# Kernel tuning notes

Hardware: AMD Instinct MI355X
Metric: run time of the kernel (lower is better)

Reference implementation:

```python
import jax, jax.numpy as jnp
import numpy as np

B, S, F, D, NH, K, NB = 128, 200, 32, 512, 4, 4, 2
Dh = D // NH
UP = 704  # round(1.3*512) up to multiple of 64
FD = 7    # forecast_days
EPS = 1e-5


def _layernorm(x, w):
    mu = x.mean(-1, keepdims=True)
    var = ((x - mu) ** 2).mean(-1, keepdims=True)
    return (x - mu) / jnp.sqrt(var + EPS) * w


def _forward(x, w_in, b_in, ln1_w, conv_w, conv_b, w_gates, r_gates, b_gates,
             gn_w, ln2_w, ff_up, ff_down, post_ln_w, fc1_w, fc1_b, fc2_w, fc2_b):
    b, s, _ = x.shape
    h = x @ w_in + b_in  # (B,S,D) input projection
    for blk in range(NB):
        xn = _layernorm(h, ln1_w[blk])
        # causal depthwise conv1d (kernel K) + swish, feeds i/f gates
        xp = jnp.pad(xn, ((0, 0), (K - 1, 0), (0, 0)))
        xc = conv_b[blk] + sum(conv_w[blk, k] * xp[:, k:k + s, :] for k in range(K))
        xc = xc * jax.nn.sigmoid(xc)  # swish
        xch = xc.reshape(b, s, NH, Dh)
        xnh = xn.reshape(b, s, NH, Dh)
        # headwise (block-diagonal) gate projections
        ipre = jnp.einsum('bshd,hde->bshe', xch, w_gates[blk, 0])
        fpre = jnp.einsum('bshd,hde->bshe', xch, w_gates[blk, 1])
        zpre = jnp.einsum('bshd,hde->bshe', xnh, w_gates[blk, 2])
        opre = jnp.einsum('bshd,hde->bshe', xnh, w_gates[blk, 3])
        pre = jnp.stack([ipre, fpre, zpre, opre], 0)        # (4,B,S,NH,Dh)
        pre = jnp.transpose(pre, (2, 0, 1, 3, 4))           # (S,4,B,NH,Dh)
        R = r_gates[blk]                                     # (4,NH,Dh,Dh)
        bg = b_gates[blk].reshape(4, NH, Dh)

        def step(carry, g):
            hs, cs, ns, ms = carry  # each (B,NH,Dh)
            rec = jnp.einsum('bhd,ghde->gbhe', hs, R)
            iraw = g[0] + rec[0] + bg[0]
            fraw = g[1] + rec[1] + bg[1]
            zraw = g[2] + rec[2] + bg[2]
            oraw = g[3] + rec[3] + bg[3]
            # stabilized exponential gating (vanilla sLSTM backend)
            logf = ms + jax.nn.log_sigmoid(fraw)
            m_new = jnp.maximum(iraw, logf)
            ig = jnp.exp(iraw - m_new)
            fg = jnp.exp(logf - m_new)
            c_new = fg * cs + ig * jnp.tanh(zraw)
            n_new = fg * ns + ig
            h_new = jax.nn.sigmoid(oraw) * c_new / n_new
            return (h_new, c_new, n_new, m_new), h_new

        z0 = jnp.zeros((b, NH, Dh), x.dtype)
        _, hseq = jax.lax.scan(step, (z0, z0, z0, z0), pre)  # (S,B,NH,Dh)
        # multi-head groupnorm (per head, over Dh)
        mu = hseq.mean(-1, keepdims=True)
        var = ((hseq - mu) ** 2).mean(-1, keepdims=True)
        y = (hseq - mu) / jnp.sqrt(var + EPS) * gn_w[blk].reshape(NH, Dh)
        y = jnp.transpose(y, (1, 0, 2, 3)).reshape(b, s, D)
        h = h + y  # residual
        # gated GeLU feedforward with residual
        xn2 = _layernorm(h, ln2_w[blk])
        u = xn2 @ ff_up[blk]                                 # (B,S,2*UP)
        gate, up = jnp.split(u, 2, -1)
        h = h + (jax.nn.gelu(gate) * up) @ ff_down[blk]
    h = _layernorm(h, post_ln_w)  # post-blocks norm
    last = h[:, -1, :]
    out = jax.nn.relu(last @ fc1_w + fc1_b) @ fc2_w + fc2_b  # (B,FD)
    return out


def setup_inputs() -> dict:
    key = jax.random.key(0)
    ks = jax.random.split(key, 12)

    def rn(k, shape, s=0.02):
        return jax.random.normal(k, shape, jnp.float32) * s

    return {
        'x': jax.random.normal(ks[0], (B, S, F), jnp.float32),
        'w_in': rn(ks[1], (F, D), 0.1),
        'b_in': jnp.zeros((D,), jnp.float32),
        'ln1_w': jnp.ones((NB, D), jnp.float32),
        'conv_w': rn(ks[2], (NB, K, D), 0.1),
        'conv_b': jnp.zeros((NB, D), jnp.float32),
        'w_gates': rn(ks[3], (NB, 4, NH, Dh, Dh), 0.05),
        'r_gates': rn(ks[4], (NB, 4, NH, Dh, Dh), 0.05),
        'b_gates': rn(ks[5], (NB, 4, D), 0.1),
        'gn_w': jnp.ones((NB, D), jnp.float32),
        'ln2_w': jnp.ones((NB, D), jnp.float32),
        'ff_up': rn(ks[6], (NB, D, 2 * UP), 0.05),
        'ff_down': rn(ks[7], (NB, UP, D), 0.05),
        'post_ln_w': jnp.ones((D,), jnp.float32),
        'fc1_w': rn(ks[8], (D, D // 2), 0.05),
        'fc1_b': jnp.zeros((D // 2,), jnp.float32),
        'fc2_w': rn(ks[9], (D // 2, FD), 0.05),
        'fc2_b': jnp.zeros((FD,), jnp.float32),
    }


def reference(x, w_in, b_in, ln1_w, conv_w, conv_b, w_gates, r_gates, b_gates,
              gn_w, ln2_w, ff_up, ff_down, post_ln_w, fc1_w, fc1_b, fc2_w, fc2_b):
    return _forward(x, w_in, b_in, ln1_w, conv_w, conv_b, w_gates, r_gates, b_gates,
                    gn_w, ln2_w, ff_up, ff_down, post_ln_w, fc1_w, fc1_b, fc2_w, fc2_b)
```

## Files before the change

### kernel.cpp

```cpp
#include <hip/hip_runtime.h>

#define B_  128
#define S_  200
#define F_  32
#define D_  512
#define NH_ 4
#define DH_ 128
#define KK_ 4
#define NB_ 2
#define UP_ 704
#define FD_ 7
#define M_  (B_*S_)

typedef unsigned short u16;
typedef _Float16 f16;
typedef __attribute__((ext_vector_type(8))) _Float16 f16x8;
typedef __attribute__((ext_vector_type(8))) short  s16x8;
typedef __attribute__((ext_vector_type(4))) float  f32x4;

__device__ __forceinline__ u16 f2bf(float f){
  unsigned x = __builtin_bit_cast(unsigned, f);
  return (u16)((x + 0x7fffu + ((x>>16)&1u)) >> 16);
}
__device__ __forceinline__ float bf2f(u16 u){
  return __builtin_bit_cast(float, (unsigned)u << 16);
}
__device__ __forceinline__ f32x4 mfma16(s16x8 a, s16x8 b, f32x4 c){
  return __builtin_amdgcn_mfma_f32_16x16x32_bf16(a, b, c, 0, 0, 0);
}
__device__ __forceinline__ f32x4 mfma16h(f16x8 a, f16x8 b, f32x4 c){
  return __builtin_amdgcn_mfma_f32_16x16x32_f16(a, b, c, 0, 0, 0);
}
__device__ __forceinline__ float frcp(float x){ return __builtin_amdgcn_rcpf(x); }
__device__ __forceinline__ float tanh_fast(float z){
  const float u = __expf(-2.f*fabsf(z));
  const float t = (1.f-u)*frcp(1.f+u);
  return copysignf(t, z);
}
__device__ __forceinline__ float logsig_fast(float f){
  const float t = __expf(-fabsf(f));
  return fminf(f, 0.f) - __logf(1.f + t);
}
__device__ __forceinline__ float sigmoid_fast(float x){
  return frcp(1.f + __expf(-x));
}
__device__ __forceinline__ void bar_lgkm(){
  __builtin_amdgcn_sched_barrier(0);
  asm volatile("s_waitcnt lgkmcnt(0)" ::: "memory");
  __builtin_amdgcn_s_barrier();
  __builtin_amdgcn_sched_barrier(0);
}
template<int CTRL>
__device__ __forceinline__ float dpp_add(float v){
  int x = __builtin_amdgcn_update_dpp(0, __builtin_bit_cast(int, v), CTRL, 0xf, 0xf, false);
  return v + __builtin_bit_cast(float, x);
}
__device__ __forceinline__ float wave_sum64(float v){
  v = dpp_add<0x111>(v);
  v = dpp_add<0x112>(v);
  v = dpp_add<0x114>(v);
  v = dpp_add<0x118>(v);
  v = dpp_add<0x142>(v);
  v = dpp_add<0x143>(v);
  return __builtin_bit_cast(float, __builtin_amdgcn_readlane(__builtin_bit_cast(int, v), 63));
}

__global__ void k_zero(float* __restrict__ p, int n){
  int i = blockIdx.x*256 + threadIdx.x;
  if (i < n) p[i] = 0.f;
}
__global__ void k_sentinel(float* __restrict__ out, int n){
  int i = blockIdx.x*256 + threadIdx.x;
  if (i < n) out[i] = -12345.0f;
}

__global__ void k_cast_pack_gates(const float* __restrict__ in, u16* __restrict__ out, int n){
  int i = blockIdx.x*256 + threadIdx.x;
  if (i >= n) return;
  const int mat = i >> 14;
  const int rem = i & 16383;
  const int slab = rem >> 12;
  const int r2   = rem & 4095;
  const int nn   = r2 >> 5;
  const int kk   = r2 & 31;
  out[i] = f2bf(in[(size_t)mat*16384 + (size_t)(slab*32 + kk)*DH_ + nn]);
}
__global__ void k_cast_pack_up(const float* __restrict__ in, u16* __restrict__ out, int n){
  int i = blockIdx.x*256 + threadIdx.x;
  if (i >= n) return;
  const int per = 512*1408;
  const int blk = i / per;
  const int rem = i - blk*per;
  const int slab = rem / (1408*32);
  const int r2   = rem - slab*(1408*32);
  const int nn   = r2 >> 5;
  const int kk   = r2 & 31;
  const int j = nn & 127, tt = nn >> 7;
  const int col = (j < 64) ? (tt*64 + j) : (UP_ + tt*64 + (j - 64));
  out[i] = f2bf(in[(size_t)(blk*512 + slab*32 + kk)*(2*UP_) + col]);
}
__global__ void k_cast_pack_dn(const float* __restrict__ in, u16* __restrict__ out, int n){
  int i = blockIdx.x*256 + threadIdx.x;
  if (i >= n) return;
  const int per = 704*512;
  const int blk = i / per;
  const int rem = i - blk*per;
  const int slab = rem / (512*32);
  const int r2   = rem - slab*(512*32);
  const int nn   = r2 >> 5;
  const int kk   = r2 & 31;
  out[i] = f2bf(in[(size_t)(blk*704 + slab*32 + kk)*D_ + nn]);
}

__global__ __launch_bounds__(256) void k_inproj(const float* __restrict__ x,
    const float* __restrict__ w, const float* __restrict__ bias, float* __restrict__ h)
{
  __shared__ float xs[8][32];
  const int m0 = blockIdx.x*8, tid = threadIdx.x;
  xs[tid>>5][tid&31] = x[(size_t)(m0 + (tid>>5))*F_ + (tid&31)];
  __syncthreads();
  #pragma unroll
  for (int hf=0; hf<2; ++hf){
    const int e = tid + hf*256;
    float a[8];
    const float bb = bias[e];
    #pragma unroll
    for (int r=0;r<8;r++) a[r]=bb;
    for (int f=0; f<F_; ++f){
      const float wv = w[(size_t)f*D_ + e];
      #pragma unroll
      for (int r=0;r<8;r++) a[r] += xs[r][f]*wv;
    }
    #pragma unroll
    for (int r=0;r<8;r++) h[(size_t)(m0+r)*D_ + e] = a[r];
  }
}

__global__ __launch_bounds__(128) void k_ln(const float* __restrict__ in, const float* __restrict__ w,
      u16* __restrict__ outb)
{
  const int row = blockIdx.x, tid = threadIdx.x;
  const f32x4* rp = (const f32x4*)(in + (size_t)row*D_);
  f32x4 v = rp[tid];
  float s = v[0]+v[1]+v[2]+v[3];
  float q = v[0]*v[0]+v[1]*v[1]+v[2]*v[2]+v[3]*v[3];
  #pragma unroll
  for (int off=32; off; off>>=1){ s += __shfl_down(s,off,64); q += __shfl_down(q,off,64); }
  __shared__ float red[2][2];
  if ((tid&63)==0){ red[tid>>6][0]=s; red[tid>>6][1]=q; }
  __syncthreads();
  const float sum = red[0][0]+red[1][0], sq = red[0][1]+red[1][1];
  const float mu  = sum*(1.f/D_);
  const float var = sq*(1.f/D_) - mu*mu;
  const float inv = rsqrtf(var + 1e-5f);
  f32x4 wv = ((const f32x4*)w)[tid];
  ushort4 ob;
  ob.x=f2bf((v[0]-mu)*inv*wv[0]); ob.y=f2bf((v[1]-mu)*inv*wv[1]);
  ob.z=f2bf((v[2]-mu)*inv*wv[2]); ob.w=f2bf((v[3]-mu)*inv*wv[3]);
  ((ushort4*)(outb + (size_t)row*D_))[tid] = ob;
}

__global__ __launch_bounds__(128) void k_addln(float* __restrict__ h, const u16* __restrict__ y,
      const float* __restrict__ w, u16* __restrict__ outb)
{
  const int row = blockIdx.x, tid = threadIdx.x;
  f32x4 v = ((const f32x4*)(h + (size_t)row*D_))[tid];
  ushort4 yq = ((const ushort4*)(y + (size_t)row*D_))[tid];
  v[0]+=bf2f(yq.x); v[1]+=bf2f(yq.y); v[2]+=bf2f(yq.z); v[3]+=bf2f(yq.w);
  ((f32x4*)(h + (size_t)row*D_))[tid] = v;
  float s = v[0]+v[1]+v[2]+v[3];
  float q = v[0]*v[0]+v[1]*v[1]+v[2]*v[2]+v[3]*v[3];
  #pragma unroll
  for (int off=32; off; off>>=1){ s += __shfl_down(s,off,64); q += __shfl_down(q,off,64); }
  __shared__ float red[2][2];
  if ((tid&63)==0){ red[tid>>6][0]=s; red[tid>>6][1]=q; }
  __syncthreads();
  const float sum = red[0][0]+red[1][0], sq = red[0][1]+red[1][1];
  const float mu  = sum*(1.f/D_);
  const float var = sq*(1.f/D_) - mu*mu;
  const float inv = rsqrtf(var + 1e-5f);
  f32x4 wv = ((const f32x4*)w)[tid];
  ushort4 ob;
  ob.x=f2bf((v[0]-mu)*inv*wv[0]); ob.y=f2bf((v[1]-mu)*inv*wv[1]);
  ob.z=f2bf((v[2]-mu)*inv*wv[2]); ob.w=f2bf((v[3]-mu)*inv*wv[3]);
  ((ushort4*)(outb + (size_t)row*D_))[tid] = ob;
}

__global__ void k_conv(const u16* __restrict__ xnbf, const float* __restrict__ cw,
                       const float* __restrict__ cb, u16* __restrict__ xcc,
                       int s0, int Sc)
{
  const int idx = blockIdx.x*256 + threadIdx.x;
  const int e4 = idx & 127;
  const int sl = (idx >> 7) % Sc;
  const int b  = idx / (128*Sc);
  const int s  = s0 + sl;
  f32x4 acc = ((const f32x4*)cb)[e4];
  #pragma unroll
  for (int k=0;k<KK_;k++){
    const int sp = s - (KK_-1) + k;
    if (sp >= 0){
      f32x4 w4 = ((const f32x4*)cw)[k*128 + e4];
      ushort4 xq = ((const ushort4*)xnbf)[(size_t)(b*S_ + sp)*128 + e4];
      acc[0] += w4[0]*bf2f(xq.x);
      acc[1] += w4[1]*bf2f(xq.y);
      acc[2] += w4[2]*bf2f(xq.z);
      acc[3] += w4[3]*bf2f(xq.w);
    }
  }
  ushort4 o;
  float a;
  a=acc[0]; o.x=f2bf(a*sigmoid_fast(a));
  a=acc[1]; o.y=f2bf(a*sigmoid_fast(a));
  a=acc[2]; o.z=f2bf(a*sigmoid_fast(a));
  a=acc[3]; o.w=f2bf(a*sigmoid_fast(a));
  ((ushort4*)xcc)[idx] = o;
}

__global__ __launch_bounds__(256) void k_gemm_ffn(
    const u16* __restrict__ A, int lda,
    const u16* __restrict__ Bw, int ldb,
    float* __restrict__ C, int ldc,
    int Kdim, int addmode)
{
  __shared__ u16 As[128*40];
  __shared__ u16 Bs[128*40];
  const int tid = threadIdx.x;
  const int m0 = blockIdx.x * 128;
  const int n0 = blockIdx.y * 128;
  const int w = tid >> 6, l = tid & 63;
  const int l16 = l & 15, kg = l >> 4;
  f32x4 acc[2][8];
  #pragma unroll
  for (int i=0;i<2;i++)
    #pragma unroll
    for (int j=0;j<8;j++) acc[i][j] = (f32x4)0.f;
  const int nk = Kdim >> 5;
  for (int kt=0; kt<nk; ++kt){
    const int k0 = kt<<5;
    __syncthreads();
    #pragma unroll
    for (int p=0;p<2;p++){
      const int idx = p*256 + tid;
      const int row = idx>>2, kc = (idx&3)*8;
      s16x8 v = *(const s16x8*)(A + (size_t)(m0+row)*lda + k0 + kc);
      *(s16x8*)&As[row*40 + kc] = v;
    }
    #pragma unroll
    for (int p=0;p<2;p++){
      const int idx = p*256 + tid;
      const int nl = idx>>2, ck = (idx&3)*8;
      s16x8 v = *(const s16x8*)(Bw + (size_t)kt*ldb*32 + (size_t)(n0+nl)*32 + ck);
      *(s16x8*)&Bs[nl*40 + ck] = v;
    }
    __syncthreads();
    s16x8 af[2];
    #pragma unroll
    for (int mf=0;mf<2;mf++)
      af[mf] = *(const s16x8*)&As[(w*32 + mf*16 + l16)*40 + kg*8];
    #pragma unroll
    for (int nf=0;nf<8;nf++){
      s16x8 bfr = *(const s16x8*)&Bs[(nf*16 + l16)*40 + kg*8];
      #pragma unroll
      for (int mf=0;mf<2;mf++)
        acc[mf][nf] = mfma16(af[mf], bfr, acc[mf][nf]);
    }
  }
  #pragma unroll
  for (int mf=0;mf<2;mf++){
    #pragma unroll
    for (int j=0;j<4;j++){
      const int row = m0 + w*32 + mf*16 + kg*4 + j;
      float* cp = C + (size_t)row*ldc + n0 + l16;
      #pragma unroll
      for (int nf=0;nf<8;nf++){
        const float v = acc[mf][nf][j];
        if (addmode) cp[nf*16] += v; else cp[nf*16] = v;
      }
    }
  }
}

__global__ __launch_bounds__(256) void k_gemm_up(
    const u16* __restrict__ A,
    const u16* __restrict__ Bw,
    u16* __restrict__ act)
{
  __shared__ u16 As[128*40];
  __shared__ u16 Bs[128*40];
  const int tid = threadIdx.x;
  const int m0 = blockIdx.x * 128;
  const int n0 = blockIdx.y * 128;
  const int w = tid >> 6, l = tid & 63;
  const int l16 = l & 15, kg = l >> 4;
  f32x4 acc[2][8];
  #pragma unroll
  for (int i=0;i<2;i++)
    #pragma unroll
    for (int j=0;j<8;j++) acc[i][j] = (f32x4)0.f;
  for (int kt=0; kt<16; ++kt){
    const int k0 = kt<<5;
    __syncthreads();
    #pragma unroll
    for (int p=0;p<2;p++){
      const int idx = p*256 + tid;
      const int row = idx>>2, kc = (idx&3)*8;
      s16x8 v = *(const s16x8*)(A + (size_t)(m0+row)*D_ + k0 + kc);
      *(s16x8*)&As[row*40 + kc] = v;
    }
    #pragma unroll
    for (int p=0;p<2;p++){
      const int idx = p*256 + tid;
      const int nl = idx>>2, ck = (idx&3)*8;
      s16x8 v = *(const s16x8*)(Bw + (size_t)kt*(2*UP_)*32 + (size_t)(n0+nl)*32 + ck);
      *(s16x8*)&Bs[nl*40 + ck] = v;
    }
    __syncthreads();
    s16x8 af[2];
    #pragma unroll
    for (int mf=0;mf<2;mf++)
      af[mf] = *(const s16x8*)&As[(w*32 + mf*16 + l16)*40 + kg*8];
    #pragma unroll
    for (int nf=0;nf<8;nf++){
      s16x8 bfr = *(const s16x8*)&Bs[(nf*16 + l16)*40 + kg*8];
      #pragma unroll
      for (int mf=0;mf<2;mf++)
        acc[mf][nf] = mfma16(af[mf], bfr, acc[mf][nf]);
    }
  }
  const int n0h = blockIdx.y * 64;
  #pragma unroll
  for (int mf=0;mf<2;mf++){
    #pragma unroll
    for (int j=0;j<4;j++){
      const int row = m0 + w*32 + mf*16 + kg*4 + j;
      u16* ap = act + (size_t)row*UP_ + n0h + l16;
      #pragma unroll
      for (int nf=0;nf<4;nf++){
        const float gg = acc[mf][nf][j];
        const float uu = acc[mf][nf+4][j];
        const float tt = tanh_fast(0.7978845608028654f*(gg + 0.044715f*gg*gg*gg));
        ap[nf*16] = f2bf(0.5f*gg*(1.f+tt)*uu);
      }
    }
  }
}

__global__ __launch_bounds__(256) void k_gemm_gates(
    const u16* __restrict__ xcc, const u16* __restrict__ xnbf,
    const u16* __restrict__ wg,
    const float* __restrict__ bgates,
    u16* __restrict__ pre, int s0, int Sc)
{
  __shared__ u16 As[128*40];
  __shared__ u16 Bs[128*40];
  const int tid = threadIdx.x;
  const int m0 = blockIdx.x * 128;
  const int gh = blockIdx.y; const int g = gh>>2, hh = gh&3;
  const u16* Bw = wg + (size_t)gh*DH_*DH_;
  const int w = tid >> 6, l = tid & 63;
  const int l16 = l & 15, kg = l >> 4;
  f32x4 acc[2][8];
  #pragma unroll
  for (int i=0;i<2;i++)
    #pragma unroll
    for (int j=0;j<8;j++) acc[i][j] = (f32x4)0.f;
  for (int kt=0; kt<4; ++kt){
    const int k0 = kt<<5;
    __syncthreads();
    #pragma unroll
    for (int p=0;p<2;p++){
      const int idx = p*256 + tid;
      const int row = idx>>2, kc = (idx&3)*8;
      const int m = m0 + row;
      size_t aoff;
      const u16* Abase;
      if (g < 2){ Abase = xcc;  aoff = (size_t)m*D_; }
      else {
        const int b2 = m / Sc, sl2 = m - b2*Sc;
        Abase = xnbf; aoff = (size_t)(b2*S_ + s0 + sl2)*D_;
      }
      s16x8 v = *(const s16x8*)(Abase + aoff + hh*DH_ + k0 + kc);
      *(s16x8*)&As[row*40 + kc] = v;
    }
    #pragma unroll
    for (int p=0;p<2;p++){
      const int idx = p*256 + tid;
      const int nl = idx>>2, ck = (idx&3)*8;
      s16x8 v = *(const s16x8*)(Bw + (size_t)kt*DH_*32 + (size_t)nl*32 + ck);
      *(s16x8*)&Bs[nl*40 + ck] = v;
    }
    __syncthreads();
    s16x8 af[2];
    #pragma unroll
    for (int mf=0;mf<2;mf++)
      af[mf] = *(const s16x8*)&As[(w*32 + mf*16 + l16)*40 + kg*8];
    #pragma unroll
    for (int nf=0;nf<8;nf++){
      s16x8 bfr = *(const s16x8*)&Bs[(nf*16 + l16)*40 + kg*8];
      #pragma unroll
      for (int mf=0;mf<2;mf++)
        acc[mf][nf] = mfma16(af[mf], bfr, acc[mf][nf]);
    }
  }
  #pragma unroll
  for (int mf=0;mf<2;mf++){
    #pragma unroll
    for (int j=0;j<4;j++){
      const int m = m0 + w*32 + mf*16 + kg*4 + j;
      const int b2 = m / Sc;
      const int sl2 = m - b2*Sc;
      #pragma unroll
      for (int nf=0;nf<8;nf++){
        const int col = nf*16 + l16;
        const float bias = bgates[g*D_ + hh*128 + col];
        pre[(((size_t)g*Sc + sl2)*B_ + b2)*D_ + hh*128 + col] =
            __builtin_bit_cast(u16, (f16)(acc[mf][nf][j] + bias));
      }
    }
  }
}

__global__ __launch_bounds__(512, 2) void k_scan(
    const u16* __restrict__ pre,
    const float* __restrict__ rg,
    const float* __restrict__ gnw,
    u16* __restrict__ ybuf,
    float* __restrict__ st, int s0, int Sc)
{
  const int t   = threadIdx.x;
  const int hh  = blockIdx.y;
  const int bg0 = blockIdx.x * 2;
  const int w   = t >> 6;
  const int l   = t & 63;
  const int g   = w >> 1;
  const int ch  = w & 1;
  const int la  = l >> 4, lb = l & 15;

  __shared__ __align__(16) char  hA[16*256];
  __shared__ __align__(16) float recl[16*132];
  __shared__ float red[2][2][2];

  f16x8 Rf[4][4];
  {
    const float* rbase = rg + ((size_t)(g*NH_ + hh)*DH_)*DH_ + ch*64;
    #pragma unroll
    for (int ct=0; ct<4; ++ct)
      #pragma unroll
      for (int ks=0; ks<4; ++ks){
        f16x8 f;
        #pragma unroll
        for (int j=0;j<8;j++)
          f[j] = (f16)rbase[(size_t)(ks*32 + la*8 + j)*DH_ + ct*16 + lb];
        Rf[ct][ks] = f;
      }
  }

  const int pb  = t >> 7;
  const int col = t & 127;
  const int wh  = (t >> 6) & 1;
  const bool act = (pb < 2);
  const int pbc = act ? pb : 0;
  const int SCMP = B_*NH_*DH_;
  const int is  = ((bg0+pbc)*NH_ + hh)*128 + col;

  for (int i = t; i < 16*128; i += 512) ((u16*)hA)[i] = 0;
  float hst=0.f, cst=0.f, nst=0.f, mst=0.f;
  if (act){
    hst = st[0*SCMP + is];
    cst = st[1*SCMP + is];
    nst = st[2*SCMP + is];
    mst = st[3*SCMP + is];
    const int slot = col >> 3;
    *(u16*)&hA[pb*256 + (((slot^pb)&15)<<4) + (col&7)*2] = __builtin_bit_cast(u16, (f16)hst);
  }
  const float gws = gnw[hh*128 + col];
  const u16* prebase = pre + (size_t)(bg0+pbc)*D_ + hh*128 + col;
  const size_t gstride = (size_t)Sc*B_*D_;
  const size_t sstride = (size_t)B_*D_;
  u16 pc16[4]={0,0,0,0}, pn16[4]={0,0,0,0};
  if (act){
    #pragma unroll
    for (int g2=0; g2<4; ++g2)
      pc16[g2] = prebase[g2*gstride];
    const int s1c = (Sc > 1) ? 1 : 0;
    #pragma unroll
    for (int g2=0; g2<4; ++g2)
      pn16[g2] = prebase[g2*gstride + (size_t)s1c*sstride];
  }
  __syncthreads();

  for (int sl=0; sl<Sc; ++sl){
    u16 pl16[4]={0,0,0,0};
    if (act){
      const int sn = (sl+2 < Sc) ? sl+2 : Sc-1;
      #pragma unroll
      for (int g2=0; g2<4; ++g2)
        pl16[g2] = prebase[g2*gstride + (size_t)sn*sstride];
    }

    f32x4 accA[4], accB[4];
    #pragma unroll
    for (int ct=0; ct<4; ++ct){ accA[ct] = (f32x4)0.f; accB[ct] = (f32x4)0.f; }
    #pragma unroll
    for (int ks=0; ks<4; ++ks){
      const int slot = ks*4 + la;
      f16x8 af = *(const f16x8*)&hA[lb*256 + (((slot ^ lb)&15)<<4)];
      if (ks < 2){
        #pragma unroll
        for (int ct=0; ct<4; ++ct) accA[ct] = mfma16h(af, Rf[ct][ks], accA[ct]);
      } else {
        #pragma unroll
        for (int ct=0; ct<4; ++ct) accB[ct] = mfma16h(af, Rf[ct][ks], accB[ct]);
      }
    }
    if (la == 0){
      #pragma unroll
      for (int ct=0; ct<4; ++ct){
        recl[(g*4 + 0)*132 + ch*64 + ct*16 + lb] = accA[ct][0] + accB[ct][0];
        recl[(g*4 + 1)*132 + ch*64 + ct*16 + lb] = accA[ct][1] + accB[ct][1];
      }
    }
    bar_lgkm();

    float hv = 0.f;
    if (act){
      const float iraw = (float)__builtin_bit_cast(f16, pc16[0]) + recl[(0*4+pb)*132 + col];
      const float fraw = (float)__builtin_bit_cast(f16, pc16[1]) + recl[(1*4+pb)*132 + col];
      const float zraw = (float)__builtin_bit_cast(f16, pc16[2]) + recl[(2*4+pb)*132 + col];
      const float oraw = (float)__builtin_bit_cast(f16, pc16[3]) + recl[(3*4+pb)*132 + col];
      const float lf   = mst + logsig_fast(fraw);
      const float mn   = fmaxf(iraw, lf);
      const float ig   = __expf(iraw - mn);
      const float fg   = __expf(lf - mn);
      cst = fg*cst + ig*tanh_fast(zraw);
      nst = fg*nst + ig;
      mst = mn;
      hv = sigmoid_fast(oraw) * cst * frcp(nst);
      hst = hv;
      const int slot = col >> 3;
      *(u16*)&hA[pb*256 + (((slot^pb)&15)<<4) + (col&7)*2] = __builtin_bit_cast(u16, (f16)hv);
      const float s1 = wave_sum64(hv);
      const float s2 = wave_sum64(hv*hv);
      if (l == 0){ red[pb][wh][0] = s1; red[pb][wh][1] = s2; }
    }
    bar_lgkm();

    if (act){
      const float sum = red[pb][0][0] + red[pb][1][0];
      const float sq  = red[pb][0][1] + red[pb][1][1];
      const float mu  = sum * (1.f/128.f);
      const float var = sq * (1.f/128.f) - mu*mu;
      const float y   = (hv - mu) * rsqrtf(var + 1e-5f) * gws;
      ybuf[((size_t)(bg0+pb)*S_ + (s0+sl))*D_ + hh*128 + col] = f2bf(y);
      pc16[0]=pn16[0]; pc16[1]=pn16[1]; pc16[2]=pn16[2]; pc16[3]=pn16[3];
      pn16[0]=pl16[0]; pn16[1]=pl16[1]; pn16[2]=pl16[2]; pn16[3]=pl16[3];
    }
  }
  if (act){
    st[0*SCMP + is] = hst;
    st[1*SCMP + is] = cst;
    st[2*SCMP + is] = nst;
    st[3*SCMP + is] = mst;
  }
}

__global__ __launch_bounds__(256) void k_head(const float* __restrict__ h,
     const float* __restrict__ pw, const float* __restrict__ f1w, const float* __restrict__ f1b,
     const float* __restrict__ f2w, const float* __restrict__ f2bias, float* __restrict__ out)
{
  const int b = blockIdx.x, tid = threadIdx.x;
  __shared__ float nrm[512];
  __shared__ float a1[256];
  __shared__ float red[4][2];
  const float* row = h + ((size_t)b*S_ + (S_-1))*D_;
  const float v0 = row[tid], v1 = row[tid+256];
  float s = v0+v1, q = v0*v0+v1*v1;
  #pragma unroll
  for (int off=32; off; off>>=1){ s += __shfl_down(s,off,64); q += __shfl_down(q,off,64); }
  if ((tid&63)==0){ red[tid>>6][0]=s; red[tid>>6][1]=q; }
  __syncthreads();
  const float sum = red[0][0]+red[1][0]+red[2][0]+red[3][0];
  const float sq  = red[0][1]+red[1][1]+red[2][1]+red[3][1];
  const float mu  = sum*(1.f/D_), var = sq*(1.f/D_) - mu*mu;
  const float inv = rsqrtf(var+1e-5f);
  nrm[tid]      = (v0-mu)*inv*pw[tid];
  nrm[tid+256]  = (v1-mu)*inv*pw[tid+256];
  __syncthreads();
  float acc = f1b[tid];
  for (int d=0; d<D_; ++d) acc += nrm[d]*f1w[(size_t)d*256 + tid];
  a1[tid] = fmaxf(acc, 0.f);
  __syncthreads();
  if (tid < FD_){
    float o = f2bias[tid];
    for (int i=0;i<256;++i) o += a1[i]*f2w[(size_t)i*FD_ + tid];
    out[b*FD_ + tid] = o;
  }
}

extern "C" void kernel_launch(void* const* d_in, const int* in_sizes, int n_in,
                              void* d_out, int out_size, void* d_ws, size_t ws_size,
                              hipStream_t stream)
{
  const float* x       = (const float*)d_in[0];
  const float* w_in    = (const float*)d_in[1];
  const float* b_in    = (const float*)d_in[2];
  const float* ln1_w   = (const float*)d_in[3];
  const float* conv_w  = (const float*)d_in[4];
  const float* conv_b  = (const float*)d_in[5];
  const float* w_gates = (const float*)d_in[6];
  const float* r_gates = (const float*)d_in[7];
  const float* b_gates = (const float*)d_in[8];
  const float* gn_w    = (const float*)d_in[9];
  const float* ln2_w   = (const float*)d_in[10];
  const float* ff_up   = (const float*)d_in[11];
  const float* ff_down = (const float*)d_in[12];
  const float* post_ln = (const float*)d_in[13];
  const float* fc1_w   = (const float*)d_in[14];
  const float* fc1_b   = (const float*)d_in[15];
  const float* fc2_w   = (const float*)d_in[16];
  const float* fc2_b   = (const float*)d_in[17];
  float* out = (float*)d_out;

  char* ws = (char*)d_ws;
  const size_t OFF_H     = 0;
  const size_t OFF_XNBF  = 52428800;
  const size_t OFF_WGBF  = 78643200;
  const size_t OFF_UPBF  = 79691776;
  const size_t OFF_DNBF  = 82575360;
  const size_t OFF_STATE = 84017152;
  const size_t OFF_YBUF  = 85065728;
  const size_t OFF_CHUNK = 111280128;

  if (ws_size < OFF_CHUNK + 655360ull){
    k_sentinel<<<4, 256, 0, stream>>>(out, out_size);
    return;
  }
  const size_t CR = ws_size - OFF_CHUNK;
  int Sc = (int)(CR / 655360ull); if (Sc > S_) Sc = S_;
  int Mc = (int)((CR / 1408ull) & ~(size_t)127); if (Mc > M_) Mc = M_;

  float* h     = (float*)(ws + OFF_H);
  u16*   xnbf  = (u16*)  (ws + OFF_XNBF);
  u16*   wgbf  = (u16*)  (ws + OFF_WGBF);
  u16*   upbf  = (u16*)  (ws + OFF_UPBF);
  u16*   dnbf  = (u16*)  (ws + OFF_DNBF);
  float* st    = (float*)(ws + OFF_STATE);
  u16*   ybuf  = (u16*)  (ws + OFF_YBUF);
  u16*   xcc   = (u16*)  (ws + OFF_CHUNK);
  u16*   prec  = (u16*)  (ws + OFF_CHUNK + (size_t)Sc*131072);
  u16*   actc  = (u16*)  (ws + OFF_CHUNK);

  {
    int n1 = NB_*4*NH_*DH_*DH_;  k_cast_pack_gates<<<(n1+255)/256, 256, 0, stream>>>(w_gates, wgbf, n1);
    int n2 = NB_*D_*2*UP_;       k_cast_pack_up<<<(n2+255)/256, 256, 0, stream>>>(ff_up, upbf, n2);
    int n3 = NB_*UP_*D_;         k_cast_pack_dn<<<(n3+255)/256, 256, 0, stream>>>(ff_down, dnbf, n3);
  }

  k_inproj<<<M_/8, 256, 0, stream>>>(x, w_in, b_in, h);

  for (int blk=0; blk<NB_; ++blk){
    k_ln<<<M_, 128, 0, stream>>>(h, ln1_w + blk*D_, xnbf);
    k_zero<<<1024, 256, 0, stream>>>(st, 4*B_*NH_*DH_);
    for (int s0=0; s0<S_; s0+=Sc){
      const int scur = (S_ - s0 < Sc) ? (S_ - s0) : Sc;
      k_conv<<<scur*64, 256, 0, stream>>>(xnbf, conv_w + blk*KK_*D_, conv_b + blk*D_,
                                          xcc, s0, scur);
      dim3 gg((B_*scur)/128, 16);
      k_gemm_gates<<<gg, 256, 0, stream>>>(xcc, xnbf,
          wgbf + (size_t)blk*4*NH_*DH_*DH_, b_gates + (size_t)blk*4*D_, prec, s0, scur);
      dim3 gs(B_/2, NH_);
      k_scan<<<gs, 512, 0, stream>>>(prec, r_gates + (size_t)blk*4*NH_*DH_*DH_,
                                     gn_w + blk*D_, ybuf, st, s0, scur);
    }
    k_addln<<<M_, 128, 0, stream>>>(h, ybuf, ln2_w + blk*D_, xnbf);
    for (int m0c=0; m0c<M_; m0c+=Mc){
      const int mcur = (M_ - m0c < Mc) ? (M_ - m0c) : Mc;
      dim3 g1(mcur/128, (2*UP_)/128);
      k_gemm_up<<<g1, 256, 0, stream>>>(xnbf + (size_t)m0c*D_,
                                        upbf + (size_t)blk*D_*2*UP_, actc);
      dim3 g2(mcur/128, D_/128);
      k_gemm_ffn<<<g2, 256, 0, stream>>>(actc, UP_,
                                         dnbf + (size_t)blk*UP_*D_, D_,
                                         h + (size_t)m0c*D_, D_, UP_, 1);
    }
  }

  k_head<<<B_, 256, 0, stream>>>(h, post_ln, fc1_w, fc1_b, fc2_w, fc2_b, out);
}
```

Baseline: 979.0 us.

## Process one batch row per scan block and double scan grid size

```diff
diff --git a/kernel.cpp b/kernel.cpp
--- a/kernel.cpp
+++ b/kernel.cpp
@@ -421,7 +421,7 @@
   }
 }
 
-__global__ __launch_bounds__(512, 2) void k_scan(
+__global__ __launch_bounds__(512, 4) void k_scan(
     const u16* __restrict__ pre,
     const float* __restrict__ rg,
     const float* __restrict__ gnw,
@@ -430,7 +430,7 @@
 {
   const int t   = threadIdx.x;
   const int hh  = blockIdx.y;
-  const int bg0 = blockIdx.x * 2;
+  const int bb  = blockIdx.x;
   const int w   = t >> 6;
   const int l   = t & 63;
   const int g   = w >> 1;
@@ -438,8 +438,8 @@
   const int la  = l >> 4, lb = l & 15;
 
   __shared__ __align__(16) char  hA[16*256];
-  __shared__ __align__(16) float recl[16*132];
-  __shared__ float red[2][2][2];
+  __shared__ __align__(16) float recl[4*132];
+  __shared__ float red[2][2];
 
   f16x8 Rf[4][4];
   {
@@ -456,13 +456,11 @@
       }
   }
 
-  const int pb  = t >> 7;
+  const bool act = (t < 128);
   const int col = t & 127;
-  const int wh  = (t >> 6) & 1;
-  const bool act = (pb < 2);
-  const int pbc = act ? pb : 0;
+  const int wh  = t >> 6;
   const int SCMP = B_*NH_*DH_;
-  const int is  = ((bg0+pbc)*NH_ + hh)*128 + col;
+  const int is  = (bb*NH_ + hh)*128 + col;
 
   for (int i = t; i < 16*128; i += 512) ((u16*)hA)[i] = 0;
   float hst=0.f, cst=0.f, nst=0.f, mst=0.f;
@@ -472,10 +470,10 @@
     nst = st[2*SCMP + is];
     mst = st[3*SCMP + is];
     const int slot = col >> 3;
-    *(u16*)&hA[pb*256 + (((slot^pb)&15)<<4) + (col&7)*2] = __builtin_bit_cast(u16, (f16)hst);
+    *(u16*)&hA[((slot&15)<<4) + (col&7)*2] = __builtin_bit_cast(u16, (f16)hst);
   }
   const float gws = gnw[hh*128 + col];
-  const u16* prebase = pre + (size_t)(bg0+pbc)*D_ + hh*128 + col;
+  const u16* prebase = pre + (size_t)bb*D_ + hh*128 + col;
   const size_t gstride = (size_t)Sc*B_*D_;
   const size_t sstride = (size_t)B_*D_;
   u16 pc16[4]={0,0,0,0}, pn16[4]={0,0,0,0};
@@ -516,19 +514,17 @@
     }
     if (la == 0){
       #pragma unroll
-      for (int ct=0; ct<4; ++ct){
-        recl[(g*4 + 0)*132 + ch*64 + ct*16 + lb] = accA[ct][0] + accB[ct][0];
-        recl[(g*4 + 1)*132 + ch*64 + ct*16 + lb] = accA[ct][1] + accB[ct][1];
-      }
+      for (int ct=0; ct<4; ++ct)
+        recl[g*132 + ch*64 + ct*16 + lb] = accA[ct][0] + accB[ct][0];
     }
     bar_lgkm();
 
     float hv = 0.f;
     if (act){
-      const float iraw = (float)__builtin_bit_cast(f16, pc16[0]) + recl[(0*4+pb)*132 + col];
-      const float fraw = (float)__builtin_bit_cast(f16, pc16[1]) + recl[(1*4+pb)*132 + col];
-      const float zraw = (float)__builtin_bit_cast(f16, pc16[2]) + recl[(2*4+pb)*132 + col];
-      const float oraw = (float)__builtin_bit_cast(f16, pc16[3]) + recl[(3*4+pb)*132 + col];
+      const float iraw = (float)__builtin_bit_cast(f16, pc16[0]) + recl[0*132 + col];
+      const float fraw = (float)__builtin_bit_cast(f16, pc16[1]) + recl[1*132 + col];
+      const float zraw = (float)__builtin_bit_cast(f16, pc16[2]) + recl[2*132 + col];
+      const float oraw = (float)__builtin_bit_cast(f16, pc16[3]) + recl[3*132 + col];
       const float lf   = mst + logsig_fast(fraw);
       const float mn   = fmaxf(iraw, lf);
       const float ig   = __expf(iraw - mn);
@@ -539,20 +535,20 @@
       hv = sigmoid_fast(oraw) * cst * frcp(nst);
       hst = hv;
       const int slot = col >> 3;
-      *(u16*)&hA[pb*256 + (((slot^pb)&15)<<4) + (col&7)*2] = __builtin_bit_cast(u16, (f16)hv);
+      *(u16*)&hA[((slot&15)<<4) + (col&7)*2] = __builtin_bit_cast(u16, (f16)hv);
       const float s1 = wave_sum64(hv);
       const float s2 = wave_sum64(hv*hv);
-      if (l == 0){ red[pb][wh][0] = s1; red[pb][wh][1] = s2; }
+      if (l == 0){ red[wh][0] = s1; red[wh][1] = s2; }
     }
     bar_lgkm();
 
     if (act){
-      const float sum = red[pb][0][0] + red[pb][1][0];
-      const float sq  = red[pb][0][1] + red[pb][1][1];
+      const float sum = red[0][0] + red[1][0];
+      const float sq  = red[0][1] + red[1][1];
       const float mu  = sum * (1.f/128.f);
       const float var = sq * (1.f/128.f) - mu*mu;
       const float y   = (hv - mu) * rsqrtf(var + 1e-5f) * gws;
-      ybuf[((size_t)(bg0+pb)*S_ + (s0+sl))*D_ + hh*128 + col] = f2bf(y);
+      ybuf[((size_t)bb*S_ + (s0+sl))*D_ + hh*128 + col] = f2bf(y);
       pc16[0]=pn16[0]; pc16[1]=pn16[1]; pc16[2]=pn16[2]; pc16[3]=pn16[3];
       pn16[0]=pl16[0]; pn16[1]=pl16[1]; pn16[2]=pl16[2]; pn16[3]=pl16[3];
     }
@@ -669,7 +665,7 @@
       dim3 gg((B_*scur)/128, 16);
       k_gemm_gates<<<gg, 256, 0, stream>>>(xcc, xnbf,
           wgbf + (size_t)blk*4*NH_*DH_*DH_, b_gates + (size_t)blk*4*D_, prec, s0, scur);
-      dim3 gs(B_/2, NH_);
+      dim3 gs(B_, NH_);
       k_scan<<<gs, 512, 0, stream>>>(prec, r_gates + (size_t)blk*4*NH_*DH_*DH_,
                                      gn_w + blk*D_, ybuf, st, s0, scur);
     }
```

Result: slower. 1.194 ms (+21.9%).
